# Kernel tuning notes

Measured on AMD Instinct MI355X. Metric: run time of the kernel, lower is better.

Reference implementation:

```python
import jax, jax.numpy as jnp
import numpy as np

N_EMBED = 1024
EMBED_DIM = 64
DECAY = 0.99
EPS = 1e-05


def setup_inputs() -> dict:
    key = jax.random.key(0)
    k1, k2 = jax.random.split(key)
    z_e = jax.random.normal(k1, (16, 4096, EMBED_DIM), dtype=jnp.float32)
    # torch init: uniform_(-1/n_embed, 1/n_embed)
    embed = (jax.random.uniform(k2, (N_EMBED, EMBED_DIM), dtype=jnp.float32) * 2.0 - 1.0) / N_EMBED
    cluster_size = jnp.zeros((N_EMBED,), dtype=jnp.float32)
    embed_avg = embed.copy()
    return {"z_e": z_e, "embed": embed, "cluster_size": cluster_size, "embed_avg": embed_avg}


def reference(z_e, embed, cluster_size, embed_avg):
    B, N, E = z_e.shape
    flat = z_e.reshape(-1, E)  # [T, E], T = B*N
    dist = (jnp.sum(flat * flat, axis=1, keepdims=True)
            - 2.0 * flat @ embed.T
            + jnp.sum(embed * embed, axis=1)[None, :])  # [T, K]
    embed_ind = jnp.argmin(dist, axis=1)  # argmax(-dist)
    z_q = embed[embed_ind].reshape(B, N, E)

    # training-mode EMA statistics (scatter-add == one-hot matmul, but memory-efficient)
    onehot_sum = jnp.zeros((N_EMBED,), flat.dtype).at[embed_ind].add(1.0)
    embed_sum = jnp.zeros((N_EMBED, E), flat.dtype).at[embed_ind].add(flat)
    new_cluster_size = DECAY * cluster_size + (1.0 - DECAY) * onehot_sum
    new_embed_avg = DECAY * embed_avg + (1.0 - DECAY) * embed_sum
    n = jnp.sum(new_cluster_size)
    cs = (new_cluster_size + EPS) / (n + N_EMBED * EPS) * n
    new_embed = new_embed_avg / cs[:, None]

    diff = jnp.mean((jax.lax.stop_gradient(z_q) - z_e) ** 2)
    z_q_st = z_e + jax.lax.stop_gradient(z_q - z_e)  # straight-through
    return (z_q_st, diff, embed_ind.reshape(B, N), new_embed, new_cluster_size, new_embed_avg)
```

## Files before the change

kernel.cpp:

```cpp
#include <hip/hip_runtime.h>
#include <math.h>

#define T_TOK 65536
#define K_CODE 1024
#define E_DIM 64
#define DECAYF 0.99f
#define EPSF 1e-5f

#define TT 256
#define QCAP 2048
#define HACC 1.3e-3f

typedef short short8 __attribute__((ext_vector_type(8)));
typedef float f32x16 __attribute__((ext_vector_type(16)));

__device__ __forceinline__ float mul_nf(float a, float b) {
#pragma clang fp contract(off)
    return a * b;
}
__device__ __forceinline__ float add_nf(float a, float b) {
#pragma clang fp contract(off)
    return a + b;
}
__device__ __forceinline__ float sub_nf(float a, float b) {
#pragma clang fp contract(off)
    return a - b;
}

__device__ __forceinline__ float np_sq_row(const float* xrow) {
    const float4* xp = reinterpret_cast<const float4*>(xrow);
    float r[8];
#pragma unroll
    for (int g = 0; g < 8; ++g) {
        float4 va = xp[2 * g], vb = xp[2 * g + 1];
        float e[8] = {va.x, va.y, va.z, va.w, vb.x, vb.y, vb.z, vb.w};
#pragma unroll
        for (int j = 0; j < 8; ++j) {
            if (g == 0) r[j] = mul_nf(e[j], e[j]);
            else        r[j] = add_nf(r[j], mul_nf(e[j], e[j]));
        }
    }
    float s01 = add_nf(r[0], r[1]);
    float s23 = add_nf(r[2], r[3]);
    float s45 = add_nf(r[4], r[5]);
    float s67 = add_nf(r[6], r[7]);
    return add_nf(add_nf(s01, s23), add_nf(s45, s67));
}

__device__ __forceinline__ unsigned f2bf_rne(float f) {
    unsigned u = __float_as_uint(f);
    u += 0x7FFFu + ((u >> 16) & 1u);
    return (u >> 16);
}

__device__ __forceinline__ void exact_key(int t0, int tl, int code, float wn,
                                          const float* __restrict__ z_e,
                                          const float* __restrict__ embed,
                                          const float* xn_s,
                                          unsigned long long* key_s) {
    const float4* xp = reinterpret_cast<const float4*>(z_e + (size_t)(t0 + tl) * E_DIM);
    const float4* wp = reinterpret_cast<const float4*>(embed + (size_t)code * E_DIM);
    float d = 0.f;
#pragma unroll
    for (int m = 0; m < 16; ++m) {
        float4 x4 = xp[m];
        float4 w4 = wp[m];
        d = __builtin_fmaf(x4.x, w4.x, d);
        d = __builtin_fmaf(x4.y, w4.y, d);
        d = __builtin_fmaf(x4.z, w4.z, d);
        d = __builtin_fmaf(x4.w, w4.w, d);
    }
    float dist = add_nf(sub_nf(xn_s[tl], d + d), wn);
    unsigned b = __float_as_uint(dist);
    unsigned mk = (b & 0x80000000u) ? ~b : (b | 0x80000000u);
    atomicMin(key_s + tl, ((unsigned long long)mk << 32) | (unsigned)code);
}


__global__ __launch_bounds__(1024) void dist_kernel(const float* __restrict__ z_e,
                                                    const float* __restrict__ embed,
                                                    float* __restrict__ out_zq,
                                                    float* __restrict__ out_ind,
                                                    float* __restrict__ diff_acc,
                                                    float* __restrict__ esum_rep,
                                                    float* __restrict__ onehot_rep,
                                                    int rep_mask) {
    __shared__ unsigned short Ws[K_CODE * E_DIM];
    __shared__ float wn_s[K_CODE];
    __shared__ float xn_s[TT];
    __shared__ float m_s[2][TT];
    __shared__ unsigned long long key_s[TT];
    __shared__ unsigned q_s[QCAP];
    __shared__ int bi_s[TT];
    __shared__ int qc_s;

    int tid = threadIdx.x;
    int lane = tid & 63;
    int wave = tid >> 6;
    int g = lane >> 5;
    int tg = wave & 7;
    int ch = wave >> 3;
    int t0 = blockIdx.x * TT;

    if (tid == 0) qc_s = 0;
    if (tid < TT) {
        key_s[tid] = ~0ull;
        xn_s[tid] = np_sq_row(z_e + (size_t)(t0 + tid) * E_DIM);
    }

    {
        int row = tid;
        const float4* wp = reinterpret_cast<const float4*>(embed + (size_t)row * E_DIM);
        uint4* WsQ = reinterpret_cast<uint4*>(Ws);
        float r8[8];
#pragma unroll
        for (int gq = 0; gq < 8; ++gq) {
            float4 va = wp[2 * gq], vb = wp[2 * gq + 1];
            float e[8] = {va.x, va.y, va.z, va.w, vb.x, vb.y, vb.z, vb.w};
#pragma unroll
            for (int j = 0; j < 8; ++j) {
                if (gq == 0) r8[j] = mul_nf(e[j], e[j]);
                else         r8[j] = add_nf(r8[j], mul_nf(e[j], e[j]));
            }
            unsigned p0 = f2bf_rne(e[0]) | (f2bf_rne(e[1]) << 16);
            unsigned p1 = f2bf_rne(e[2]) | (f2bf_rne(e[3]) << 16);
            unsigned p2 = f2bf_rne(e[4]) | (f2bf_rne(e[5]) << 16);
            unsigned p3 = f2bf_rne(e[6]) | (f2bf_rne(e[7]) << 16);
            WsQ[row * 8 + (gq ^ (row & 7))] = make_uint4(p0, p1, p2, p3);
        }
        float s01 = add_nf(r8[0], r8[1]);
        float s23 = add_nf(r8[2], r8[3]);
        float s45 = add_nf(r8[4], r8[5]);
        float s67 = add_nf(r8[6], r8[7]);
        wn_s[row] = add_nf(add_nf(s01, s23), add_nf(s45, s67));
    }

    int arow = tg * 32 + (lane & 31);
    const float* xrow = z_e + (size_t)(t0 + arow) * E_DIM;
    short8 afr[4];
#pragma unroll
    for (int kc = 0; kc < 4; ++kc) {
        int base = kc * 16 + g * 8;
        float4 a = *reinterpret_cast<const float4*>(xrow + base);
        float4 b = *reinterpret_cast<const float4*>(xrow + base + 4);
        afr[kc][0] = (short)f2bf_rne(a.x);
        afr[kc][1] = (short)f2bf_rne(a.y);
        afr[kc][2] = (short)f2bf_rne(a.z);
        afr[kc][3] = (short)f2bf_rne(a.w);
        afr[kc][4] = (short)f2bf_rne(b.x);
        afr[kc][5] = (short)f2bf_rne(b.y);
        afr[kc][6] = (short)f2bf_rne(b.z);
        afr[kc][7] = (short)f2bf_rne(b.w);
    }

    __syncthreads();

    float maxr[16];
#pragma unroll
    for (int r = 0; r < 16; ++r) maxr[r] = -INFINITY;

#pragma unroll 2
    for (int tt = 0; tt < 16; ++tt) {
        int code = (ch * 16 + tt) * 32 + (lane & 31);
        f32x16 acc;
#pragma unroll
        for (int i = 0; i < 16; ++i) acc[i] = 0.f;
#pragma unroll
        for (int kc = 0; kc < 4; ++kc) {
            int ps = (2 * kc + g) ^ (code & 7);
            short8 bfr = *reinterpret_cast<const short8*>(&Ws[code * E_DIM + ps * 8]);
            acc = __builtin_amdgcn_mfma_f32_32x32x16_bf16(afr[kc], bfr, acc, 0, 0, 0);
        }
#pragma unroll
        for (int r = 0; r < 16; ++r) maxr[r] = fmaxf(maxr[r], acc[r]);
    }

#pragma unroll
    for (int off = 1; off < 32; off <<= 1) {
#pragma unroll
        for (int r = 0; r < 16; ++r)
            maxr[r] = fmaxf(maxr[r], __shfl_xor(maxr[r], off, 64));
    }
    if ((lane & 31) == 0) {
#pragma unroll
        for (int r = 0; r < 16; ++r) {
            int row = (r & 3) + 8 * (r >> 2) + 4 * g;
            m_s[ch][tg * 32 + row] = maxr[r];
        }
    }
    __syncthreads();

#pragma unroll
    for (int r = 0; r < 16; ++r) {
        int row = (r & 3) + 8 * (r >> 2) + 4 * g;
        int tok = tg * 32 + row;
        maxr[r] = fmaxf(m_s[0][tok], m_s[1][tok]) - HACC;
    }

#pragma unroll 2
    for (int tt = 0; tt < 16; ++tt) {
        int code = (ch * 16 + tt) * 32 + (lane & 31);
        f32x16 acc;
#pragma unroll
        for (int i = 0; i < 16; ++i) acc[i] = 0.f;
#pragma unroll
        for (int kc = 0; kc < 4; ++kc) {
            int ps = (2 * kc + g) ^ (code & 7);
            short8 bfr = *reinterpret_cast<const short8*>(&Ws[code * E_DIM + ps * 8]);
            acc = __builtin_amdgcn_mfma_f32_32x32x16_bf16(afr[kc], bfr, acc, 0, 0, 0);
        }
        float tmax = -INFINITY;
#pragma unroll
        for (int r = 0; r < 16; ++r) tmax = fmaxf(tmax, acc[r] - maxr[r]);
        if (tmax >= 0.f) {
#pragma unroll
            for (int r = 0; r < 16; ++r) {
                if (acc[r] >= maxr[r]) {
                    int row = (r & 3) + 8 * (r >> 2) + 4 * g;
                    int tl = tg * 32 + row;
                    int slot = atomicAdd(&qc_s, 1);
                    if (slot < QCAP)
                        q_s[slot] = ((unsigned)tl << 10) | (unsigned)code;
                    else
                        exact_key(t0, tl, code, wn_s[code], z_e, embed, xn_s, key_s);
                }
            }
        }
    }
    __syncthreads();

    int qn = qc_s;
    if (qn > QCAP) qn = QCAP;
    for (int e = tid; e < qn; e += 1024) {
        unsigned q = q_s[e];
        int tl = (int)(q >> 10);
        int code = (int)(q & 1023u);
        exact_key(t0, tl, code, wn_s[code], z_e, embed, xn_s, key_s);
    }
    __syncthreads();

    if (tid < TT) {
        int bi = (int)(unsigned)(key_s[tid] & 1023ull);
        bi_s[tid] = bi;
        out_ind[t0 + tid] = (float)bi;
    }
    __syncthreads();

    int rep = blockIdx.x & rep_mask;
    float* esum = esum_rep + (size_t)rep * (K_CODE * E_DIM);
    float* onehot = onehot_rep + (size_t)rep * K_CODE;

    float ds = 0.f;
#pragma unroll 4
    for (int it = 0; it < 16; ++it) {
        int tl = wave * 16 + it;
        int bi = bi_s[tl];
        float xv = z_e[(size_t)(t0 + tl) * E_DIM + lane];
        float wv = embed[(size_t)bi * E_DIM + lane];
        float rr = sub_nf(wv, xv);
        out_zq[(size_t)(t0 + tl) * E_DIM + lane] = add_nf(xv, rr);
        ds = __builtin_fmaf(rr, rr, ds);
        atomicAdd(&esum[(size_t)bi * E_DIM + lane], xv);
        if (lane == 0) atomicAdd(&onehot[bi], 1.0f);
    }
#pragma unroll
    for (int o = 32; o > 0; o >>= 1) ds += __shfl_down(ds, o, 64);
    if (lane == 0) atomicAdd(diff_acc, ds);
}

__global__ __launch_bounds__(256) void finalize_kernel(const float* __restrict__ cluster_size,
                                                       const float* __restrict__ onehot_rep,
                                                       const float* __restrict__ ws_diff,
                                                       const float* __restrict__ embed_avg,
                                                       const float* __restrict__ esum_rep,
                                                       float* __restrict__ out_diff,
                                                       float* __restrict__ out_ncs,
                                                       float* __restrict__ out_ne,
                                                       float* __restrict__ out_nea,
                                                       int nrep) {
    __shared__ float ncs_s[K_CODE];
    __shared__ float red[K_CODE];
    int tid = threadIdx.x;

#pragma unroll
    for (int i = 0; i < 4; ++i) {
        int k = tid + 256 * i;
        float oh = 0.f;
        for (int r = 0; r < nrep; ++r) oh += onehot_rep[(size_t)r * K_CODE + k];
        float ncs = DECAYF * cluster_size[k] + (1.0f - DECAYF) * oh;
        ncs_s[k] = ncs;
        red[k] = ncs;
    }
    __syncthreads();
    for (int s = 512; s > 0; s >>= 1) {
        for (int idx = tid; idx < s; idx += 256) red[idx] += red[idx + s];
        __syncthreads();
    }
    float n = red[0];

    if (blockIdx.x == 0) {
#pragma unroll
        for (int i = 0; i < 4; ++i) {
            int k = tid + 256 * i;
            out_ncs[k] = ncs_s[k];
        }
        if (tid == 0) out_diff[0] = ws_diff[0] * (1.0f / 4194304.0f);
    }

    int k = blockIdx.x * 16 + (tid >> 4);
    int c = tid & 15;
    float ncs = ncs_s[k];
    float cs = (ncs + EPSF) / (n + (float)K_CODE * EPSF) * n;

    size_t off = (size_t)k * E_DIM + (size_t)c * 4;
    float4 s4 = make_float4(0.f, 0.f, 0.f, 0.f);
    for (int r = 0; r < nrep; ++r) {
        float4 v = *reinterpret_cast<const float4*>(esum_rep + (size_t)r * (K_CODE * E_DIM) + off);
        s4.x += v.x; s4.y += v.y; s4.z += v.z; s4.w += v.w;
    }
    float4 a = *reinterpret_cast<const float4*>(embed_avg + off);
    float4 nea, ne;
    nea.x = DECAYF * a.x + (1.0f - DECAYF) * s4.x;
    nea.y = DECAYF * a.y + (1.0f - DECAYF) * s4.y;
    nea.z = DECAYF * a.z + (1.0f - DECAYF) * s4.z;
    nea.w = DECAYF * a.w + (1.0f - DECAYF) * s4.w;
    ne.x = nea.x / cs; ne.y = nea.y / cs; ne.z = nea.z / cs; ne.w = nea.w / cs;
    *reinterpret_cast<float4*>(out_nea + off) = nea;
    *reinterpret_cast<float4*>(out_ne + off) = ne;
}

extern "C" void kernel_launch(void* const* d_in, const int* in_sizes, int n_in,
                              void* d_out, int out_size, void* d_ws, size_t ws_size,
                              hipStream_t stream) {
    const float* z_e = (const float*)d_in[0];
    const float* embed = (const float*)d_in[1];
    const float* cluster_size = (const float*)d_in[2];
    const float* embed_avg = (const float*)d_in[3];

    float* out = (float*)d_out;
    float* o_zq = out;
    float* o_diff = out + 4194304;
    float* o_ind = out + 4194305;
    float* o_ne = out + 4194305 + 65536;
    float* o_ncs = o_ne + 65536;
    float* o_nea = o_ncs + 1024;

    float* ws = (float*)d_ws;
    float* ws_diff = ws + 0;
    float* ws_onehot = ws + 16;

    int nrep = 1;
    while (nrep < 8 &&
           (size_t)(8208 + (size_t)(2 * nrep) * 65536) * sizeof(float) <= ws_size)
        nrep *= 2;

    float* ws_esum = ws + 8208;

    hipMemsetAsync(ws, 0, (size_t)(8208 + (size_t)nrep * 65536) * sizeof(float), stream);

    dist_kernel<<<T_TOK / TT, 1024, 0, stream>>>(z_e, embed, o_zq, o_ind, ws_diff,
                                                 ws_esum, ws_onehot, nrep - 1);
    finalize_kernel<<<64, 256, 0, stream>>>(cluster_size, ws_onehot, ws_diff, embed_avg,
                                            ws_esum, o_diff, o_ncs, o_ne, o_nea, nrep);
}
```

Before: 210.2 us.

## Merge two MFMA passes into a single pass with a running max threshold

The block shrinks from 1024 to 512 threads. Each wave now owns 32 tokens and sweeps all 1024 codes itself, so the code space is no longer split across two wave groups. The separate max pass and the candidate pass become one pass: the running max is refreshed with a cross-lane reduction every 4 tiles and used as the candidate threshold. This halves the MFMA work and removes a block barrier and the shared max exchange. The cost is half the waves per block, and early thresholds are looser, so more candidates are queued for exact rescoring (QCAP is doubled to hold them).

```diff
diff --git a/kernel.cpp b/kernel.cpp
--- a/kernel.cpp
+++ b/kernel.cpp
@@ -8,7 +8,7 @@
 #define EPSF 1e-5f
 
 #define TT 256
-#define QCAP 2048
+#define QCAP 4096
 #define HACC 1.3e-3f
 
 typedef short short8 __attribute__((ext_vector_type(8)));
@@ -77,18 +77,17 @@
 }
 
 
-__global__ __launch_bounds__(1024) void dist_kernel(const float* __restrict__ z_e,
-                                                    const float* __restrict__ embed,
-                                                    float* __restrict__ out_zq,
-                                                    float* __restrict__ out_ind,
-                                                    float* __restrict__ diff_acc,
-                                                    float* __restrict__ esum_rep,
-                                                    float* __restrict__ onehot_rep,
-                                                    int rep_mask) {
+__global__ __launch_bounds__(512) void dist_kernel(const float* __restrict__ z_e,
+                                                   const float* __restrict__ embed,
+                                                   float* __restrict__ out_zq,
+                                                   float* __restrict__ out_ind,
+                                                   float* __restrict__ diff_acc,
+                                                   float* __restrict__ esum_rep,
+                                                   float* __restrict__ onehot_rep,
+                                                   int rep_mask) {
     __shared__ unsigned short Ws[K_CODE * E_DIM];
     __shared__ float wn_s[K_CODE];
     __shared__ float xn_s[TT];
-    __shared__ float m_s[2][TT];
     __shared__ unsigned long long key_s[TT];
     __shared__ unsigned q_s[QCAP];
     __shared__ int bi_s[TT];
@@ -98,8 +97,6 @@
     int lane = tid & 63;
     int wave = tid >> 6;
     int g = lane >> 5;
-    int tg = wave & 7;
-    int ch = wave >> 3;
     int t0 = blockIdx.x * TT;
 
     if (tid == 0) qc_s = 0;
@@ -108,8 +105,9 @@
         xn_s[tid] = np_sq_row(z_e + (size_t)(t0 + tid) * E_DIM);
     }
 
-    {
-        int row = tid;
+#pragma unroll
+    for (int rr = 0; rr < 2; ++rr) {
+        int row = tid + rr * 512;
         const float4* wp = reinterpret_cast<const float4*>(embed + (size_t)row * E_DIM);
         uint4* WsQ = reinterpret_cast<uint4*>(Ws);
         float r8[8];
@@ -135,7 +133,7 @@
         wn_s[row] = add_nf(add_nf(s01, s23), add_nf(s45, s67));
     }
 
-    int arow = tg * 32 + (lane & 31);
+    int arow = wave * 32 + (lane & 31);
     const float* xrow = z_e + (size_t)(t0 + arow) * E_DIM;
     short8 afr[4];
 #pragma unroll
@@ -155,13 +153,13 @@
 
     __syncthreads();
 
-    float maxr[16];
+    float maxr[16], thr[16];
 #pragma unroll
     for (int r = 0; r < 16; ++r) maxr[r] = -INFINITY;
 
-#pragma unroll 2
-    for (int tt = 0; tt < 16; ++tt) {
-        int code = (ch * 16 + tt) * 32 + (lane & 31);
+#pragma unroll 4
+    for (int tile = 0; tile < 32; ++tile) {
+        int code = tile * 32 + (lane & 31);
         f32x16 acc;
 #pragma unroll
         for (int i = 0; i < 16; ++i) acc[i] = 0.f;
@@ -173,51 +171,25 @@
         }
 #pragma unroll
         for (int r = 0; r < 16; ++r) maxr[r] = fmaxf(maxr[r], acc[r]);
-    }
-
-#pragma unroll
-    for (int off = 1; off < 32; off <<= 1) {
-#pragma unroll
-        for (int r = 0; r < 16; ++r)
-            maxr[r] = fmaxf(maxr[r], __shfl_xor(maxr[r], off, 64));
-    }
-    if ((lane & 31) == 0) {
-#pragma unroll
-        for (int r = 0; r < 16; ++r) {
-            int row = (r & 3) + 8 * (r >> 2) + 4 * g;
-            m_s[ch][tg * 32 + row] = maxr[r];
-        }
-    }
-    __syncthreads();
-
-#pragma unroll
-    for (int r = 0; r < 16; ++r) {
-        int row = (r & 3) + 8 * (r >> 2) + 4 * g;
-        int tok = tg * 32 + row;
-        maxr[r] = fmaxf(m_s[0][tok], m_s[1][tok]) - HACC;
-    }
-
-#pragma unroll 2
-    for (int tt = 0; tt < 16; ++tt) {
-        int code = (ch * 16 + tt) * 32 + (lane & 31);
-        f32x16 acc;
-#pragma unroll
-        for (int i = 0; i < 16; ++i) acc[i] = 0.f;
-#pragma unroll
-        for (int kc = 0; kc < 4; ++kc) {
-            int ps = (2 * kc + g) ^ (code & 7);
-            short8 bfr = *reinterpret_cast<const short8*>(&Ws[code * E_DIM + ps * 8]);
-            acc = __builtin_amdgcn_mfma_f32_32x32x16_bf16(afr[kc], bfr, acc, 0, 0, 0);
+        if ((tile & 3) == 0) {
+#pragma unroll
+            for (int off = 1; off < 32; off <<= 1) {
+#pragma unroll
+                for (int r = 0; r < 16; ++r)
+                    maxr[r] = fmaxf(maxr[r], __shfl_xor(maxr[r], off, 64));
+            }
+#pragma unroll
+            for (int r = 0; r < 16; ++r) thr[r] = maxr[r] - HACC;
         }
         float tmax = -INFINITY;
 #pragma unroll
-        for (int r = 0; r < 16; ++r) tmax = fmaxf(tmax, acc[r] - maxr[r]);
+        for (int r = 0; r < 16; ++r) tmax = fmaxf(tmax, acc[r] - thr[r]);
         if (tmax >= 0.f) {
 #pragma unroll
             for (int r = 0; r < 16; ++r) {
-                if (acc[r] >= maxr[r]) {
+                if (acc[r] >= thr[r]) {
                     int row = (r & 3) + 8 * (r >> 2) + 4 * g;
-                    int tl = tg * 32 + row;
+                    int tl = wave * 32 + row;
                     int slot = atomicAdd(&qc_s, 1);
                     if (slot < QCAP)
                         q_s[slot] = ((unsigned)tl << 10) | (unsigned)code;
@@ -231,7 +203,7 @@
 
     int qn = qc_s;
     if (qn > QCAP) qn = QCAP;
-    for (int e = tid; e < qn; e += 1024) {
+    for (int e = tid; e < qn; e += 512) {
         unsigned q = q_s[e];
         int tl = (int)(q >> 10);
         int code = (int)(q & 1023u);
@@ -252,8 +224,8 @@
 
     float ds = 0.f;
 #pragma unroll 4
-    for (int it = 0; it < 16; ++it) {
-        int tl = wave * 16 + it;
+    for (int it = 0; it < 32; ++it) {
+        int tl = wave * 32 + it;
         int bi = bi_s[tl];
         float xv = z_e[(size_t)(t0 + tl) * E_DIM + lane];
         float wv = embed[(size_t)bi * E_DIM + lane];
@@ -358,8 +330,8 @@
 
     hipMemsetAsync(ws, 0, (size_t)(8208 + (size_t)nrep * 65536) * sizeof(float), stream);
 
-    dist_kernel<<<T_TOK / TT, 1024, 0, stream>>>(z_e, embed, o_zq, o_ind, ws_diff,
-                                                 ws_esum, ws_onehot, nrep - 1);
+    dist_kernel<<<T_TOK / TT, 512, 0, stream>>>(z_e, embed, o_zq, o_ind, ws_diff,
+                                                ws_esum, ws_onehot, nrep - 1);
     finalize_kernel<<<64, 256, 0, stream>>>(cluster_size, ws_onehot, ws_diff, embed_avg,
                                             ws_esum, o_diff, o_ncs, o_ne, o_nea, nrep);
 }
```

New measurement: 224.0 us. +6.5%, slower.
